# Kernel optimization log

Measured on AMD Instinct MI355X. Metric: run time of the kernel, lower is better.

The kernel has to match this reference:

```python
import jax, jax.numpy as jnp
import numpy as np

NUM_NODES_PER_GRAPH = 24
NUM_EDGES_PER_GRAPH = 76
NUM_GRAPHS = 8192
HIDDEN = 128
NODE_F = 16
EDGE_F = 8
N_LAYERS = 4


def setup_inputs() -> dict:
    key = jax.random.key(0)
    ks = jax.random.split(key, 16)
    N = NUM_NODES_PER_GRAPH * NUM_GRAPHS
    E = NUM_EDGES_PER_GRAPH * NUM_GRAPHS
    x = jax.random.normal(ks[0], (N, NODE_F), dtype=jnp.float32)
    edge_attr = jax.random.normal(ks[1], (E, EDGE_F), dtype=jnp.float32)
    # per-graph random topology, offset by graph id so edges stay within graphs
    base = jax.random.randint(ks[2], (2, NUM_EDGES_PER_GRAPH), 0, NUM_NODES_PER_GRAPH)
    offs = (jnp.arange(NUM_GRAPHS) * NUM_NODES_PER_GRAPH)[None, :, None]  # [1,B,1]
    edge_index = (base[:, None, :] + offs).reshape(2, E).astype(jnp.int64)
    batch = jnp.repeat(jnp.arange(NUM_GRAPHS), NUM_NODES_PER_GRAPH).astype(jnp.int64)
    s = 1.0 / np.sqrt(HIDDEN)
    W_node = jax.random.normal(ks[3], (NODE_F, HIDDEN), dtype=jnp.float32) * (1.0 / np.sqrt(NODE_F))
    b_node = jnp.zeros((HIDDEN,), jnp.float32)
    W_edge = jax.random.normal(ks[4], (EDGE_F + NUM_EDGES_PER_GRAPH, HIDDEN), dtype=jnp.float32) * 0.1
    b_edge = jnp.zeros((HIDDEN,), jnp.float32)
    W_conv = jax.random.normal(ks[5], (N_LAYERS, HIDDEN, HIDDEN), dtype=jnp.float32) * s
    b_conv = jnp.zeros((N_LAYERS, HIDDEN), jnp.float32)
    W_res = jax.random.normal(ks[6], (HIDDEN, HIDDEN), dtype=jnp.float32) * s
    b_res = jnp.zeros((HIDDEN,), jnp.float32)
    W_dec = jax.random.normal(ks[7], (3 * HIDDEN, 1), dtype=jnp.float32) * (1.0 / np.sqrt(3 * HIDDEN))
    b_dec = jnp.zeros((1,), jnp.float32)
    return {"x": x, "edge_index": edge_index, "edge_attr": edge_attr, "batch": batch,
            "W_node": W_node, "b_node": b_node, "W_edge": W_edge, "b_edge": b_edge,
            "W_conv": W_conv, "b_conv": b_conv, "W_res": W_res, "b_res": b_res,
            "W_dec": W_dec, "b_dec": b_dec}


def _gcn_conv(x, W, b, row, col, norm, num_nodes):
    # PyG GCNConv: symmetric-normalized aggregation (with self-loops) of x @ W, plus bias.
    h = x @ W  # [N, H]
    msg = h[row] * norm[:, None]  # gather source, scale
    out = jax.ops.segment_sum(msg, col, num_segments=num_nodes)
    return out + b


def _forward(x, edge_index, edge_attr, W_node, b_node, W_edge, b_edge,
             W_conv, b_conv, W_res, b_res, W_dec, b_dec):
    N = x.shape[0]
    E = edge_attr.shape[0]
    row, col = edge_index[0], edge_index[1]

    # ---- encoder ----
    x_enc = jax.nn.relu(x @ W_node + b_node)
    # edge encoder: cat([edge_attr, tiled eye(76)]) @ W_edge == edge_attr @ W_edge[:F]
    # + row-gather of W_edge[F:] by position-within-graph (avoids materializing the eye tile)
    edge_pos = jnp.arange(E) % NUM_EDGES_PER_GRAPH
    e_enc = jax.nn.relu(edge_attr @ W_edge[:EDGE_F] + W_edge[EDGE_F:][edge_pos] + b_edge)

    # ---- gcn_norm with self-loops (shared across layers) ----
    loops = jnp.arange(N)
    row_sl = jnp.concatenate([row, loops])
    col_sl = jnp.concatenate([col, loops])
    deg = jax.ops.segment_sum(jnp.ones_like(col_sl, dtype=x.dtype), col_sl, num_segments=N)
    dinv = jax.lax.rsqrt(deg)
    norm = dinv[row_sl] * dinv[col_sl]

    # ---- GNN layers: relu(conv(x) + residual(x)) ----
    h = x_enc
    for l in range(W_conv.shape[0]):
        conv = _gcn_conv(h, W_conv[l], b_conv[l], row_sl, col_sl, norm, N)
        h = jax.nn.relu(conv + (h @ W_res + b_res))

    # ---- decoder: gather endpoints, concat edge emb, tiny linear ----
    H = h.shape[1]
    # cat([h[row], h[col], e_enc]) @ W_dec done as three small matmuls (no [E,3H] buffer)
    out = (h[row] @ W_dec[:H] + h[col] @ W_dec[H:2 * H] + e_enc @ W_dec[2 * H:] + b_dec)
    return out[:, 0]


def reference(x, edge_index, edge_attr, batch, W_node, b_node, W_edge, b_edge,
              W_conv, b_conv, W_res, b_res, W_dec, b_dec):
    return _forward(x, edge_index, edge_attr, W_node, b_node, W_edge, b_edge,
                    W_conv, b_conv, W_res, b_res, W_dec, b_dec)
```

## Files before the change

### kernel.cpp

```cpp
#include <hip/hip_runtime.h>

typedef short bf16x8 __attribute__((ext_vector_type(8)));
typedef float f32x4  __attribute__((ext_vector_type(4)));

#define N_NODES 24
#define N_EDGES 76
#define N_GRAPHS 8192
#define HID 128
#define NODE_F 16
#define EDGE_F 8
#define TOT_E (N_EDGES * N_GRAPHS)
#define ST 136
#define TT 56
#define AST 72
#define GPB 2
#define M 48

__global__ void k_pattern(const int* __restrict__ ei, unsigned short* __restrict__ Ag)
{
    __shared__ float A[N_NODES][N_NODES];
    __shared__ int cnt[N_NODES];
    __shared__ float dinv[N_NODES];
    const int t = threadIdx.x;
    for (int i = t; i < N_NODES * N_NODES; i += 128) ((float*)A)[i] = 0.f;
    if (t < N_NODES) cnt[t] = 0;
    __syncthreads();
    if (t < N_EDGES) atomicAdd(&cnt[ei[TOT_E + t]], 1);
    __syncthreads();
    if (t < N_NODES) dinv[t] = rsqrtf((float)(cnt[t] + 1));
    __syncthreads();
    if (t < N_EDGES) {
        const int r = ei[t], c = ei[TOT_E + t];
        atomicAdd(&A[c][r], dinv[r] * dinv[c]);
    }
    __syncthreads();
    if (t < N_NODES) A[t][t] += dinv[t] * dinv[t];
    __syncthreads();
    for (int i = t; i < M * AST; i += 128) {
        const int row = i / AST, k = i - row * AST;
        float v = 0.f;
        if (row < N_NODES) { if (k < N_NODES) v = A[row][k]; }
        else if (k >= N_NODES && k < 2 * N_NODES) v = A[row - N_NODES][k - N_NODES];
        const unsigned int u = __float_as_uint(v);
        const unsigned short hi = (unsigned short)(u >> 16);
        const float hf = __uint_as_float(u & 0xFFFF0000u);
        const unsigned short lo = (unsigned short)(__float_as_uint(v - hf) >> 16);
        Ag[i] = hi;
        Ag[M * AST + i] = lo;
    }
}

__global__ __launch_bounds__(256) void k_wprep(
    const float* __restrict__ Wcv, const float* __restrict__ Wr,
    unsigned short* __restrict__ whi, unsigned short* __restrict__ wlo)
{
    int idx = blockIdx.x * 256 + threadIdx.x;
    int m = idx >> 14, rem = idx & 16383;
    int k = rem >> 7, c = rem & 127;
    const float* src = (m < 4) ? (Wcv + m * 16384) : Wr;
    float x = src[k * HID + c];
    unsigned int u = __float_as_uint(x);
    unsigned short hi = (unsigned short)(u >> 16);
    float hf = __uint_as_float(u & 0xFFFF0000u);
    unsigned short lo = (unsigned short)(__float_as_uint(x - hf) >> 16);
    whi[m * 16384 + c * HID + k] = hi;
    wlo[m * 16384 + c * HID + k] = lo;
}

__device__ __forceinline__ void split2(float xv, unsigned short& hs, unsigned short& ls)
{
    unsigned int u = __float_as_uint(xv);
    hs = (unsigned short)(u >> 16);
    float hf = __uint_as_float(u & 0xFFFF0000u);
    ls = (unsigned short)(__float_as_uint(xv - hf) >> 16);
}

struct Smem {
    unsigned short planes[2][M * ST];
    unsigned short ttT[2][128 * TT + 8];
    unsigned short Ap[2][M * AST];
};

__global__ __launch_bounds__(512, 4) void k_fused(
    const float* __restrict__ x, const float* __restrict__ Wn,
    const float* __restrict__ bn,
    const unsigned short* __restrict__ whi, const unsigned short* __restrict__ wlo,
    const unsigned short* __restrict__ Ag,
    const float* __restrict__ bcv, const float* __restrict__ br,
    const int* __restrict__ ei, const float* __restrict__ ea,
    const float* __restrict__ We, const float* __restrict__ be,
    const float* __restrict__ Wd, const float* __restrict__ bd,
    float* __restrict__ out)
{
    __shared__ Smem s;
    const int t = threadIdx.x;
    const int w = t >> 6, l = t & 63;
    const int lr = l & 15, lq = l >> 4;
    const int col16 = 16 * w + lr;
    const int hcb = 16 * w + 4 * lq;
    const int wko = col16 * HID + 8 * lq;

    bf16x8 Wrh[4];
#pragma unroll
    for (int ks = 0; ks < 4; ++ks)
        Wrh[ks] = *(const bf16x8*)(whi + 4 * 16384 + wko + 32 * ks);
    const float4 br4 = *(const float4*)(br + hcb);

    const long long n0 = (long long)blockIdx.x * M;
    if (t < 192) ((float4*)s.ttT)[t] = ((const float4*)(x + n0 * NODE_F))[t];
    {
        const uint4* src = (const uint4*)Ag;
        uint4* dst = (uint4*)s.Ap;
#pragma unroll 2
        for (int i = t; i < 2 * M * AST / 8; i += 512) dst[i] = src[i];
    }
    __syncthreads();

    {
        const int c = t & 127, tq = t >> 7;
        float wn[NODE_F];
#pragma unroll
        for (int k = 0; k < NODE_F; ++k) wn[k] = Wn[k * HID + c];
        const float bnc = bn[c];
        const float* xt = (const float*)s.ttT;
#pragma unroll
        for (int jj = 0; jj < 12; ++jj) {
            const int n = tq * 12 + jj;
            float acc = bnc;
#pragma unroll
            for (int k = 0; k < NODE_F; ++k) acc = fmaf(xt[n * NODE_F + k], wn[k], acc);
            acc = fmaxf(acc, 0.f);
            unsigned short hs, ls;
            split2(acc, hs, ls);
            s.planes[0][n * ST + c] = hs;
            s.planes[1][n * ST + c] = ls;
        }
    }
    __syncthreads();

    if (t < 256) {
        *(uint4*)&s.ttT[t >> 7][(t & 127) * TT + 48] = make_uint4(0u, 0u, 0u, 0u);
    } else if (t < 258) {
        *(uint4*)&s.ttT[t - 256][128 * TT] = make_uint4(0u, 0u, 0u, 0u);
    }

    for (int lyr = 0; lyr < 4; ++lyr) {
        bf16x8 Wch[4];
#pragma unroll
        for (int ks = 0; ks < 4; ++ks)
            Wch[ks] = *(const bf16x8*)(whi + lyr * 16384 + wko + 32 * ks);
        const float4 bc4 = *(const float4*)(bcv + lyr * HID + hcb);

        f32x4 accT[3], accRT[3];
#pragma unroll
        for (int mt = 0; mt < 3; ++mt) {
            accT[mt]  = (f32x4){0.f, 0.f, 0.f, 0.f};
            accRT[mt] = (f32x4){0.f, 0.f, 0.f, 0.f};
        }
#pragma unroll
        for (int ks = 0; ks < 4; ++ks) {
            const int ko = 32 * ks + 8 * lq;
            const bf16x8 Wcl = *(const bf16x8*)(wlo + lyr * 16384 + wko + 32 * ks);
            const bf16x8 Wrl = *(const bf16x8*)(wlo + 4 * 16384 + wko + 32 * ks);
            bf16x8 ahi[3];
#pragma unroll
            for (int mt = 0; mt < 3; ++mt) {
                const int row16 = 16 * mt + lr;
                ahi[mt] = *(const bf16x8*)&s.planes[0][row16 * ST + ko];
                const bf16x8 alo = *(const bf16x8*)&s.planes[1][row16 * ST + ko];
                accT[mt]  = __builtin_amdgcn_mfma_f32_16x16x32_bf16(ahi[mt], Wch[ks], accT[mt], 0, 0, 0);
                accT[mt]  = __builtin_amdgcn_mfma_f32_16x16x32_bf16(alo, Wch[ks], accT[mt], 0, 0, 0);
                accRT[mt] = __builtin_amdgcn_mfma_f32_16x16x32_bf16(Wrh[ks], ahi[mt], accRT[mt], 0, 0, 0);
                accRT[mt] = __builtin_amdgcn_mfma_f32_16x16x32_bf16(Wrh[ks], alo, accRT[mt], 0, 0, 0);
            }
#pragma unroll
            for (int mt = 0; mt < 3; ++mt) {
                accT[mt]  = __builtin_amdgcn_mfma_f32_16x16x32_bf16(ahi[mt], Wcl, accT[mt], 0, 0, 0);
                accRT[mt] = __builtin_amdgcn_mfma_f32_16x16x32_bf16(Wrl, ahi[mt], accRT[mt], 0, 0, 0);
            }
        }

#pragma unroll
        for (int mt = 0; mt < 3; ++mt) {
            unsigned short hs[4], ls[4];
#pragma unroll
            for (int j = 0; j < 4; ++j) split2(accT[mt][j], hs[j], ls[j]);
            *(ushort4*)&s.ttT[0][col16 * TT + 16 * mt + 4 * lq] = make_ushort4(hs[0], hs[1], hs[2], hs[3]);
            *(ushort4*)&s.ttT[1][col16 * TT + 16 * mt + 4 * lq] = make_ushort4(ls[0], ls[1], ls[2], ls[3]);
        }
        __syncthreads();

        bf16x8 Th[2], Tl[2];
#pragma unroll
        for (int ks = 0; ks < 2; ++ks) {
            Th[ks] = *(const bf16x8*)&s.ttT[0][col16 * TT + 32 * ks + 8 * lq];
            Tl[ks] = *(const bf16x8*)&s.ttT[1][col16 * TT + 32 * ks + 8 * lq];
        }
        f32x4 accF[3];
#pragma unroll
        for (int nt = 0; nt < 3; ++nt) {
            const int brow = (16 * nt + lr) * AST + 8 * lq;
            accF[nt] = accRT[nt];
#pragma unroll
            for (int ks = 0; ks < 2; ++ks) {
                const bf16x8 Bh = *(const bf16x8*)&s.Ap[0][brow + 32 * ks];
                const bf16x8 Bl = *(const bf16x8*)&s.Ap[1][brow + 32 * ks];
                accF[nt] = __builtin_amdgcn_mfma_f32_16x16x32_bf16(Th[ks], Bh, accF[nt], 0, 0, 0);
                accF[nt] = __builtin_amdgcn_mfma_f32_16x16x32_bf16(Tl[ks], Bh, accF[nt], 0, 0, 0);
                accF[nt] = __builtin_amdgcn_mfma_f32_16x16x32_bf16(Th[ks], Bl, accF[nt], 0, 0, 0);
            }
        }

#pragma unroll
        for (int nt = 0; nt < 3; ++nt) {
            const int node = 16 * nt + lr;
            unsigned short hs[4], ls[4];
            const float bb[4] = {bc4.x + br4.x, bc4.y + br4.y, bc4.z + br4.z, bc4.w + br4.w};
#pragma unroll
            for (int j = 0; j < 4; ++j) {
                float v = fmaxf(accF[nt][j] + bb[j], 0.f);
                split2(v, hs[j], ls[j]);
            }
            *(ushort4*)&s.planes[0][node * ST + hcb] = make_ushort4(hs[0], hs[1], hs[2], hs[3]);
            *(ushort4*)&s.planes[1][node * ST + hcb] = make_ushort4(ls[0], ls[1], ls[2], ls[3]);
        }
        __syncthreads();
    }

    {
        const int c0 = l, c1 = l + 64;
        float wef0[8], wef1[8];
#pragma unroll
        for (int f = 0; f < 8; ++f) {
            wef0[f] = We[f * HID + c0];
            wef1[f] = We[f * HID + c1];
        }
        const float wd00 = Wd[c0], wd01 = Wd[c1];
        const float wd10 = Wd[HID + c0], wd11 = Wd[HID + c1];
        const float wd20 = Wd[2 * HID + c0], wd21 = Wd[2 * HID + c1];
        const float be0 = be[c0], be1 = be[c1], bd0 = bd[0];
        for (int it = 0; it < 19; ++it) {
            const int e_loc = 19 * w + it;
            const int gl = (e_loc >= 76) ? 1 : 0;
            const int j = e_loc - 76 * gl;
            const int g = blockIdx.x * GPB + gl;
            const int e = g * N_EDGES + j;
            const int nrow = ei[e] - g * N_NODES;
            const int ncol = ei[TOT_E + e] - g * N_NODES;
            const float4 a0 = *(const float4*)(ea + (size_t)e * EDGE_F);
            const float4 a1 = *(const float4*)(ea + (size_t)e * EDGE_F + 4);
            float enc0 = be0 + We[(EDGE_F + j) * HID + c0];
            float enc1 = be1 + We[(EDGE_F + j) * HID + c1];
            enc0 = fmaf(a0.x, wef0[0], enc0); enc1 = fmaf(a0.x, wef1[0], enc1);
            enc0 = fmaf(a0.y, wef0[1], enc0); enc1 = fmaf(a0.y, wef1[1], enc1);
            enc0 = fmaf(a0.z, wef0[2], enc0); enc1 = fmaf(a0.z, wef1[2], enc1);
            enc0 = fmaf(a0.w, wef0[3], enc0); enc1 = fmaf(a0.w, wef1[3], enc1);
            enc0 = fmaf(a1.x, wef0[4], enc0); enc1 = fmaf(a1.x, wef1[4], enc1);
            enc0 = fmaf(a1.y, wef0[5], enc0); enc1 = fmaf(a1.y, wef1[5], enc1);
            enc0 = fmaf(a1.z, wef0[6], enc0); enc1 = fmaf(a1.z, wef1[6], enc1);
            enc0 = fmaf(a1.w, wef0[7], enc0); enc1 = fmaf(a1.w, wef1[7], enc1);
            enc0 = fmaxf(enc0, 0.f); enc1 = fmaxf(enc1, 0.f);
            float v = enc0 * wd20 + enc1 * wd21;
            const int rr = gl * N_NODES + nrow, rc = gl * N_NODES + ncol;
            float hr0 = __uint_as_float((unsigned int)s.planes[0][rr * ST + c0] << 16)
                      + __uint_as_float((unsigned int)s.planes[1][rr * ST + c0] << 16);
            float hr1 = __uint_as_float((unsigned int)s.planes[0][rr * ST + c1] << 16)
                      + __uint_as_float((unsigned int)s.planes[1][rr * ST + c1] << 16);
            float hc0 = __uint_as_float((unsigned int)s.planes[0][rc * ST + c0] << 16)
                      + __uint_as_float((unsigned int)s.planes[1][rc * ST + c0] << 16);
            float hc1 = __uint_as_float((unsigned int)s.planes[0][rc * ST + c1] << 16)
                      + __uint_as_float((unsigned int)s.planes[1][rc * ST + c1] << 16);
            v = fmaf(hr0, wd00, v);
            v = fmaf(hr1, wd01, v);
            v = fmaf(hc0, wd10, v);
            v = fmaf(hc1, wd11, v);
#pragma unroll
            for (int o = 32; o > 0; o >>= 1) v += __shfl_xor(v, o, 64);
            if (l == 0) out[e] = v + bd0;
        }
    }
}

extern "C" void kernel_launch(void* const* d_in, const int* in_sizes, int n_in,
                              void* d_out, int out_size, void* d_ws, size_t ws_size,
                              hipStream_t stream) {
    const float* x   = (const float*)d_in[0];
    const int*   ei  = (const int*)d_in[1];
    const float* ea  = (const float*)d_in[2];
    const float* Wn  = (const float*)d_in[4];
    const float* bn  = (const float*)d_in[5];
    const float* We  = (const float*)d_in[6];
    const float* be  = (const float*)d_in[7];
    const float* Wcv = (const float*)d_in[8];
    const float* bcv = (const float*)d_in[9];
    const float* Wr  = (const float*)d_in[10];
    const float* br  = (const float*)d_in[11];
    const float* Wd  = (const float*)d_in[12];
    const float* bd  = (const float*)d_in[13];
    float* out = (float*)d_out;

    char* ws = (char*)d_ws;
    unsigned short* whi = (unsigned short*)ws;
    unsigned short* wlo = whi + 5 * 16384;
    unsigned short* Ag  = wlo + 5 * 16384;

    k_pattern<<<1, 128, 0, stream>>>(ei, Ag);
    k_wprep<<<5 * 16384 / 256, 256, 0, stream>>>(Wcv, Wr, whi, wlo);
    k_fused<<<N_GRAPHS / GPB, 512, 0, stream>>>(x, Wn, bn, whi, wlo, Ag, bcv, br,
                                                ei, ea, We, be, Wd, bd, out);
}
```

Measured before the change: 321.6 us.

## Precompute per-node decoder projections and split edge-encoder term into separate kernel

The decoder is restructured so each node's final hidden state is projected onto the row and column decoder weights once, and each edge then only adds two per-node scalars plus a precomputed edge term. The edge-encoder contribution is computed in a new standalone kernel that writes a per-edge buffer. The node encoder is moved onto bf16 MFMA with a hi/lo split of the inputs and weights. This removes the per-edge 128-wide reductions inside the fused kernel, at the cost of an extra kernel launch and a round trip of the edge buffer through global memory.

Measured after the change: 359.1 us. +11.7%, slower.

```diff
diff --git a/kernel.cpp b/kernel.cpp
--- a/kernel.cpp
+++ b/kernel.cpp
@@ -15,6 +15,8 @@
 #define AST 72
 #define GPB 2
 #define M 48
+#define WN_OFF (5 * 16384)
+#define W_ELEMS (5 * 16384 + 128 * 32)
 
 __global__ void k_pattern(const int* __restrict__ ei, unsigned short* __restrict__ Ag)
 {
@@ -52,19 +54,60 @@
 
 __global__ __launch_bounds__(256) void k_wprep(
     const float* __restrict__ Wcv, const float* __restrict__ Wr,
+    const float* __restrict__ Wn,
     unsigned short* __restrict__ whi, unsigned short* __restrict__ wlo)
 {
     int idx = blockIdx.x * 256 + threadIdx.x;
-    int m = idx >> 14, rem = idx & 16383;
-    int k = rem >> 7, c = rem & 127;
-    const float* src = (m < 4) ? (Wcv + m * 16384) : Wr;
-    float x = src[k * HID + c];
+    if (idx >= W_ELEMS) return;
+    float x; int dst;
+    if (idx < 5 * 16384) {
+        int m = idx >> 14, rem = idx & 16383;
+        int k = rem >> 7, c = rem & 127;
+        const float* src = (m < 4) ? (Wcv + m * 16384) : Wr;
+        x = src[k * HID + c];
+        dst = m * 16384 + c * HID + k;
+    } else {
+        int rem = idx - 5 * 16384;
+        int c = rem >> 5, k = rem & 31;
+        x = (k < NODE_F) ? Wn[k * HID + c] : 0.f;
+        dst = WN_OFF + c * 32 + k;
+    }
     unsigned int u = __float_as_uint(x);
     unsigned short hi = (unsigned short)(u >> 16);
     float hf = __uint_as_float(u & 0xFFFF0000u);
     unsigned short lo = (unsigned short)(__float_as_uint(x - hf) >> 16);
-    whi[m * 16384 + c * HID + k] = hi;
-    wlo[m * 16384 + c * HID + k] = lo;
+    whi[dst] = hi;
+    wlo[dst] = lo;
+}
+
+__global__ __launch_bounds__(256) void k_edgeq(
+    const float* __restrict__ ea, const float* __restrict__ We,
+    const float* __restrict__ be, const float* __restrict__ Wd,
+    const float* __restrict__ bd, float* __restrict__ qbuf)
+{
+    const int wv = threadIdx.x >> 6, l = threadIdx.x & 63;
+    const int e = blockIdx.x * 4 + wv;
+    const int j = e % N_EDGES;
+    const float4 a0 = *(const float4*)(ea + (size_t)e * EDGE_F);
+    const float4 a1 = *(const float4*)(ea + (size_t)e * EDGE_F + 4);
+    float part = 0.f;
+#pragma unroll
+    for (int u = 0; u < 2; ++u) {
+        const int c = l + 64 * u;
+        float enc = be[c] + We[(EDGE_F + j) * HID + c];
+        enc = fmaf(a0.x, We[0 * HID + c], enc);
+        enc = fmaf(a0.y, We[1 * HID + c], enc);
+        enc = fmaf(a0.z, We[2 * HID + c], enc);
+        enc = fmaf(a0.w, We[3 * HID + c], enc);
+        enc = fmaf(a1.x, We[4 * HID + c], enc);
+        enc = fmaf(a1.y, We[5 * HID + c], enc);
+        enc = fmaf(a1.z, We[6 * HID + c], enc);
+        enc = fmaf(a1.w, We[7 * HID + c], enc);
+        part = fmaf(fmaxf(enc, 0.f), Wd[2 * HID + c], part);
+    }
+#pragma unroll
+    for (int o = 32; o > 0; o >>= 1) part += __shfl_xor(part, o, 64);
+    if (l == 0) qbuf[e] = part + bd[0];
 }
 
 __device__ __forceinline__ void split2(float xv, unsigned short& hs, unsigned short& ls)
@@ -82,15 +125,12 @@
 };
 
 __global__ __launch_bounds__(512, 4) void k_fused(
-    const float* __restrict__ x, const float* __restrict__ Wn,
-    const float* __restrict__ bn,
+    const float* __restrict__ x, const float* __restrict__ bn,
     const unsigned short* __restrict__ whi, const unsigned short* __restrict__ wlo,
     const unsigned short* __restrict__ Ag,
     const float* __restrict__ bcv, const float* __restrict__ br,
-    const int* __restrict__ ei, const float* __restrict__ ea,
-    const float* __restrict__ We, const float* __restrict__ be,
-    const float* __restrict__ Wd, const float* __restrict__ bd,
-    float* __restrict__ out)
+    const int* __restrict__ ei, const float* __restrict__ Wd,
+    const float* __restrict__ qbuf, float* __restrict__ out)
 {
     __shared__ Smem s;
     const int t = threadIdx.x;
@@ -107,7 +147,28 @@
     const float4 br4 = *(const float4*)(br + hcb);
 
     const long long n0 = (long long)blockIdx.x * M;
-    if (t < 192) ((float4*)s.ttT)[t] = ((const float4*)(x + n0 * NODE_F))[t];
+    {
+        const float* xg = x + n0 * NODE_F;
+        {
+            const int e = t;
+            unsigned short hs, ls;
+            split2(xg[e], hs, ls);
+            s.ttT[0][(e >> 4) * 32 + (e & 15)] = hs;
+            s.ttT[1][(e >> 4) * 32 + (e & 15)] = ls;
+        }
+        if (t < 256) {
+            const int e = 512 + t;
+            unsigned short hs, ls;
+            split2(xg[e], hs, ls);
+            s.ttT[0][(e >> 4) * 32 + (e & 15)] = hs;
+            s.ttT[1][(e >> 4) * 32 + (e & 15)] = ls;
+        }
+        if (t < 384) {
+            const int p = t / 192, i = t % 192;
+            const int row = i >> 2, jj = i & 3;
+            *(ushort4*)&s.ttT[p][row * 32 + 16 + 4 * jj] = make_ushort4(0, 0, 0, 0);
+        }
+    }
     {
         const uint4* src = (const uint4*)Ag;
         uint4* dst = (uint4*)s.Ap;
@@ -117,23 +178,32 @@
     __syncthreads();
 
     {
-        const int c = t & 127, tq = t >> 7;
-        float wn[NODE_F];
-#pragma unroll
-        for (int k = 0; k < NODE_F; ++k) wn[k] = Wn[k * HID + c];
-        const float bnc = bn[c];
-        const float* xt = (const float*)s.ttT;
-#pragma unroll
-        for (int jj = 0; jj < 12; ++jj) {
-            const int n = tq * 12 + jj;
-            float acc = bnc;
-#pragma unroll
-            for (int k = 0; k < NODE_F; ++k) acc = fmaf(xt[n * NODE_F + k], wn[k], acc);
-            acc = fmaxf(acc, 0.f);
-            unsigned short hs, ls;
-            split2(acc, hs, ls);
-            s.planes[0][n * ST + c] = hs;
-            s.planes[1][n * ST + c] = ls;
+        const bf16x8 Wnh = *(const bf16x8*)(whi + WN_OFF + col16 * 32 + 8 * lq);
+        const bf16x8 Wnl = *(const bf16x8*)(wlo + WN_OFF + col16 * 32 + 8 * lq);
+        const float4 bn4 = *(const float4*)(bn + hcb);
+        f32x4 accE[3];
+#pragma unroll
+        for (int nt = 0; nt < 3; ++nt) accE[nt] = (f32x4){0.f, 0.f, 0.f, 0.f};
+#pragma unroll
+        for (int nt = 0; nt < 3; ++nt) {
+            const bf16x8 xh = *(const bf16x8*)&s.ttT[0][(16 * nt + lr) * 32 + 8 * lq];
+            const bf16x8 xl = *(const bf16x8*)&s.ttT[1][(16 * nt + lr) * 32 + 8 * lq];
+            accE[nt] = __builtin_amdgcn_mfma_f32_16x16x32_bf16(Wnh, xh, accE[nt], 0, 0, 0);
+            accE[nt] = __builtin_amdgcn_mfma_f32_16x16x32_bf16(Wnh, xl, accE[nt], 0, 0, 0);
+            accE[nt] = __builtin_amdgcn_mfma_f32_16x16x32_bf16(Wnl, xh, accE[nt], 0, 0, 0);
+        }
+#pragma unroll
+        for (int nt = 0; nt < 3; ++nt) {
+            const int node = 16 * nt + lr;
+            unsigned short hs[4], ls[4];
+            const float bb[4] = {bn4.x, bn4.y, bn4.z, bn4.w};
+#pragma unroll
+            for (int j = 0; j < 4; ++j) {
+                float v = fmaxf(accE[nt][j] + bb[j], 0.f);
+                split2(v, hs[j], ls[j]);
+            }
+            *(ushort4*)&s.planes[0][node * ST + hcb] = make_ushort4(hs[0], hs[1], hs[2], hs[3]);
+            *(ushort4*)&s.planes[1][node * ST + hcb] = make_ushort4(ls[0], ls[1], ls[2], ls[3]);
         }
     }
     __syncthreads();
@@ -211,72 +281,57 @@
             }
         }
 
-#pragma unroll
-        for (int nt = 0; nt < 3; ++nt) {
-            const int node = 16 * nt + lr;
-            unsigned short hs[4], ls[4];
-            const float bb[4] = {bc4.x + br4.x, bc4.y + br4.y, bc4.z + br4.z, bc4.w + br4.w};
-#pragma unroll
-            for (int j = 0; j < 4; ++j) {
-                float v = fmaxf(accF[nt][j] + bb[j], 0.f);
-                split2(v, hs[j], ls[j]);
-            }
-            *(ushort4*)&s.planes[0][node * ST + hcb] = make_ushort4(hs[0], hs[1], hs[2], hs[3]);
-            *(ushort4*)&s.planes[1][node * ST + hcb] = make_ushort4(ls[0], ls[1], ls[2], ls[3]);
-        }
-        __syncthreads();
-    }
-
-    {
-        const int c0 = l, c1 = l + 64;
-        float wef0[8], wef1[8];
-#pragma unroll
-        for (int f = 0; f < 8; ++f) {
-            wef0[f] = We[f * HID + c0];
-            wef1[f] = We[f * HID + c1];
-        }
-        const float wd00 = Wd[c0], wd01 = Wd[c1];
-        const float wd10 = Wd[HID + c0], wd11 = Wd[HID + c1];
-        const float wd20 = Wd[2 * HID + c0], wd21 = Wd[2 * HID + c1];
-        const float be0 = be[c0], be1 = be[c1], bd0 = bd[0];
-        for (int it = 0; it < 19; ++it) {
-            const int e_loc = 19 * w + it;
-            const int gl = (e_loc >= 76) ? 1 : 0;
-            const int j = e_loc - 76 * gl;
-            const int g = blockIdx.x * GPB + gl;
-            const int e = g * N_EDGES + j;
-            const int nrow = ei[e] - g * N_NODES;
-            const int ncol = ei[TOT_E + e] - g * N_NODES;
-            const float4 a0 = *(const float4*)(ea + (size_t)e * EDGE_F);
-            const float4 a1 = *(const float4*)(ea + (size_t)e * EDGE_F + 4);
-            float enc0 = be0 + We[(EDGE_F + j) * HID + c0];
-            float enc1 = be1 + We[(EDGE_F + j) * HID + c1];
-            enc0 = fmaf(a0.x, wef0[0], enc0); enc1 = fmaf(a0.x, wef1[0], enc1);
-            enc0 = fmaf(a0.y, wef0[1], enc0); enc1 = fmaf(a0.y, wef1[1], enc1);
-            enc0 = fmaf(a0.z, wef0[2], enc0); enc1 = fmaf(a0.z, wef1[2], enc1);
-            enc0 = fmaf(a0.w, wef0[3], enc0); enc1 = fmaf(a0.w, wef1[3], enc1);
-            enc0 = fmaf(a1.x, wef0[4], enc0); enc1 = fmaf(a1.x, wef1[4], enc1);
-            enc0 = fmaf(a1.y, wef0[5], enc0); enc1 = fmaf(a1.y, wef1[5], enc1);
-            enc0 = fmaf(a1.z, wef0[6], enc0); enc1 = fmaf(a1.z, wef1[6], enc1);
-            enc0 = fmaf(a1.w, wef0[7], enc0); enc1 = fmaf(a1.w, wef1[7], enc1);
-            enc0 = fmaxf(enc0, 0.f); enc1 = fmaxf(enc1, 0.f);
-            float v = enc0 * wd20 + enc1 * wd21;
-            const int rr = gl * N_NODES + nrow, rc = gl * N_NODES + ncol;
-            float hr0 = __uint_as_float((unsigned int)s.planes[0][rr * ST + c0] << 16)
-                      + __uint_as_float((unsigned int)s.planes[1][rr * ST + c0] << 16);
-            float hr1 = __uint_as_float((unsigned int)s.planes[0][rr * ST + c1] << 16)
-                      + __uint_as_float((unsigned int)s.planes[1][rr * ST + c1] << 16);
-            float hc0 = __uint_as_float((unsigned int)s.planes[0][rc * ST + c0] << 16)
-                      + __uint_as_float((unsigned int)s.planes[1][rc * ST + c0] << 16);
-            float hc1 = __uint_as_float((unsigned int)s.planes[0][rc * ST + c1] << 16)
-                      + __uint_as_float((unsigned int)s.planes[1][rc * ST + c1] << 16);
-            v = fmaf(hr0, wd00, v);
-            v = fmaf(hr1, wd01, v);
-            v = fmaf(hc0, wd10, v);
-            v = fmaf(hc1, wd11, v);
-#pragma unroll
-            for (int o = 32; o > 0; o >>= 1) v += __shfl_xor(v, o, 64);
-            if (l == 0) out[e] = v + bd0;
+        const float bb[4] = {bc4.x + br4.x, bc4.y + br4.y, bc4.z + br4.z, bc4.w + br4.w};
+        if (lyr < 3) {
+#pragma unroll
+            for (int nt = 0; nt < 3; ++nt) {
+                const int node = 16 * nt + lr;
+                unsigned short hs[4], ls[4];
+#pragma unroll
+                for (int j = 0; j < 4; ++j) {
+                    float v = fmaxf(accF[nt][j] + bb[j], 0.f);
+                    split2(v, hs[j], ls[j]);
+                }
+                *(ushort4*)&s.planes[0][node * ST + hcb] = make_ushort4(hs[0], hs[1], hs[2], hs[3]);
+                *(ushort4*)&s.planes[1][node * ST + hcb] = make_ushort4(ls[0], ls[1], ls[2], ls[3]);
+            }
+            __syncthreads();
+        } else {
+            float* pred = (float*)s.planes;
+            const float4 wd0 = *(const float4*)(Wd + hcb);
+            const float4 wd1 = *(const float4*)(Wd + HID + hcb);
+            const int chunk = 4 * w + lq;
+#pragma unroll
+            for (int nt = 0; nt < 3; ++nt) {
+                const int node = 16 * nt + lr;
+                float h0 = fmaxf(accF[nt][0] + bb[0], 0.f);
+                float h1 = fmaxf(accF[nt][1] + bb[1], 0.f);
+                float h2 = fmaxf(accF[nt][2] + bb[2], 0.f);
+                float h3 = fmaxf(accF[nt][3] + bb[3], 0.f);
+                float p0 = h0 * wd0.x + h1 * wd0.y + h2 * wd0.z + h3 * wd0.w;
+                float p1 = h0 * wd1.x + h1 * wd1.y + h2 * wd1.z + h3 * wd1.w;
+                pred[node * 33 + chunk] = p0;
+                pred[(48 + node) * 33 + chunk] = p1;
+            }
+            __syncthreads();
+            float* pv = pred + 96 * 33;
+            if (t < 96) {
+                const float* rowp = pred + t * 33;
+                float sum = 0.f;
+#pragma unroll
+                for (int i = 0; i < 32; ++i) sum += rowp[i];
+                pv[t] = sum;
+            }
+            __syncthreads();
+            if (t < 2 * N_EDGES) {
+                const int gl = (t >= N_EDGES) ? 1 : 0;
+                const int j = t - N_EDGES * gl;
+                const int g = blockIdx.x * GPB + gl;
+                const int e = g * N_EDGES + j;
+                const int nrow = ei[e] - g * N_NODES + gl * N_NODES;
+                const int ncol = ei[TOT_E + e] - g * N_NODES + gl * N_NODES;
+                out[e] = pv[nrow] + pv[48 + ncol] + qbuf[e];
+            }
         }
     }
 }
@@ -301,11 +356,13 @@
 
     char* ws = (char*)d_ws;
     unsigned short* whi = (unsigned short*)ws;
-    unsigned short* wlo = whi + 5 * 16384;
-    unsigned short* Ag  = wlo + 5 * 16384;
+    unsigned short* wlo = whi + W_ELEMS;
+    unsigned short* Ag  = wlo + W_ELEMS;
+    float* qbuf = (float*)(Ag + 2 * M * AST);
 
     k_pattern<<<1, 128, 0, stream>>>(ei, Ag);
-    k_wprep<<<5 * 16384 / 256, 256, 0, stream>>>(Wcv, Wr, whi, wlo);
-    k_fused<<<N_GRAPHS / GPB, 512, 0, stream>>>(x, Wn, bn, whi, wlo, Ag, bcv, br,
-                                                ei, ea, We, be, Wd, bd, out);
-}
+    k_wprep<<<(W_ELEMS + 255) / 256, 256, 0, stream>>>(Wcv, Wr, Wn, whi, wlo);
+    k_edgeq<<<TOT_E / 4, 256, 0, stream>>>(ea, We, be, Wd, bd, qbuf);
+    k_fused<<<N_GRAPHS / GPB, 512, 0, stream>>>(x, bn, whi, wlo, Ag, bcv, br,
+                                                ei, Wd, qbuf, out);
+}
```
